# Kernel optimization log

Measured on AMD Instinct MI355X. Metric: run time of the kernel, lower is better.

## Reference

```python
import jax, jax.numpy as jnp
import numpy as np

N_NODES = 50000
N_HEADS = 8


def _make_edges(n, e_rand, seed=0):
    # unique random edges + self-loops so every row has >=1 neighbor
    rng = np.random.default_rng(seed)
    flat = rng.integers(0, n * n, size=e_rand, dtype=np.int64)
    flat = np.unique(np.concatenate([flat, np.arange(n, dtype=np.int64) * (n + 1)]))
    src = (flat // n).astype(np.int32)
    dst = (flat % n).astype(np.int32)
    return jnp.stack([jnp.asarray(src), jnp.asarray(dst)])


def setup_inputs() -> dict:
    key = jax.random.key(0)
    ks = jax.random.split(key, 10)
    d_in, d_att, d_out = 256, 64, 256
    dph = d_out // N_HEADS  # 32, per-head output dim of linearW
    s = 0.05
    return {
        "features": jax.random.normal(ks[0], (N_NODES, d_in), jnp.float32),
        "edge_index": _make_edges(N_NODES, 1_600_000),
        "Wq": jax.random.normal(ks[1], (N_HEADS, d_att, d_in), jnp.float32) * s,
        "bq": jax.random.normal(ks[2], (N_HEADS, d_att), jnp.float32) * s,
        "Wk": jax.random.normal(ks[3], (N_HEADS, d_att, d_in), jnp.float32) * s,
        "bk": jax.random.normal(ks[4], (N_HEADS, d_att), jnp.float32) * s,
        "Ww": jax.random.normal(ks[5], (dph, d_in), jnp.float32) * s,
        "bw": jax.random.normal(ks[6], (dph,), jnp.float32) * s,
        "Wb": jax.random.normal(ks[7], (d_out, d_in), jnp.float32) * s,
        "bb": jax.random.normal(ks[8], (d_out,), jnp.float32) * s,
    }


def reference(features, edge_index, Wq, bq, Wk, bk, Ww, bw, Wb, bb):
    n = features.shape[0]
    src, dst = edge_index[0], edge_index[1]
    # shared value projection (linearW is one layer reused for all heads)
    V = features @ Ww.T + bw  # [N, dph]
    head_outs = []
    for h in range(N_HEADS):  # structural loop over heads, as in the original
        q = features @ Wq[h].T + bq[h]  # [N, d_att]
        k = features @ Wk[h].T + bk[h]  # [N, d_att]
        s = jnp.sum(q[src] * k[dst], axis=-1)  # [E] = scores[i,j]=q_i.k_j on edges
        # row-wise (per source node) softmax over neighbors == dense masked softmax
        smax = jax.ops.segment_max(s, src, num_segments=n)
        ex = jnp.exp(s - jax.lax.stop_gradient(smax)[src])
        denom = jax.ops.segment_sum(ex, src, num_segments=n)
        alpha = ex / denom[src]  # [E]
        head_outs.append(jax.ops.segment_sum(alpha[:, None] * V[dst], src, num_segments=n))
    agg = jnp.concatenate(head_outs, axis=1)  # [N, d_out]
    return features @ Wb.T + bb + agg
```

## Files before the change

### kernel.cpp

```cpp
#include <hip/hip_runtime.h>
#include <hip/hip_fp16.h>

typedef _Float16 f16;
typedef _Float16 f16x2 __attribute__((ext_vector_type(2)));
typedef _Float16 f16x8 __attribute__((ext_vector_type(8)));
typedef float f32x4 __attribute__((ext_vector_type(4)));

#define WC_ROWS 1312
#define WC_PAD 1408

__global__ void prep_weights(const float* __restrict__ Wq, const float* __restrict__ bq,
                             const float* __restrict__ Wk, const float* __restrict__ bk,
                             const float* __restrict__ Ww, const float* __restrict__ bw,
                             const float* __restrict__ Wb, const float* __restrict__ bb,
                             f16* __restrict__ Wc, float* __restrict__ bias) {
    int id = blockIdx.x * 256 + threadIdx.x;
    int j = id >> 8, k = id & 255;
    if (j >= WC_PAD) return;
    float v;
    if (j < 512)       v = Wq[j*256 + k];
    else if (j < 1024) v = Wk[(j-512)*256 + k];
    else if (j < 1056) v = Ww[(j-1024)*256 + k];
    else if (j < 1312) v = Wb[(j-1056)*256 + k];
    else               v = 0.f;
    Wc[j*256 + k] = (f16)v;
    if (k == 0) {
        float b;
        if (j < 512)       b = bq[j];
        else if (j < 1024) b = bk[j-512];
        else if (j < 1056) b = bw[j-1024];
        else if (j < 1312) b = bb[j-1056];
        else               b = 0.f;
        bias[j] = b;
    }
}

__global__ void build_rows(const int* __restrict__ src, int E, int n, int* __restrict__ rs) {
    int e = blockIdx.x * 256 + threadIdx.x;
    if (e == 0) rs[n] = E;
    if (e < E) {
        if (e == 0 || src[e] != src[e-1]) rs[src[e]] = e;
    }
}

__device__ __forceinline__ int swz_slot(int row, int c) {
    return row * 4 + (c ^ (row & 3) ^ ((row >> 2) & 3));
}

__device__ __forceinline__ uint4 cvt8(float4 a, float4 b) {
    f16x8 o;
    o[0] = (f16)a.x; o[1] = (f16)a.y; o[2] = (f16)a.z; o[3] = (f16)a.w;
    o[4] = (f16)b.x; o[5] = (f16)b.y; o[6] = (f16)b.z; o[7] = (f16)b.w;
    return __builtin_bit_cast(uint4, o);
}

__launch_bounds__(256)
__global__ void gemm_fused(const float* __restrict__ F, const f16* __restrict__ Wc,
                           const float* __restrict__ bias,
                           f16* __restrict__ Qb, f16* __restrict__ Kb, f16* __restrict__ Vb,
                           float* __restrict__ Out, int n) {
    __shared__ uint4 As4[512];
    __shared__ uint4 Bs4[512];
    int t = threadIdx.x;
    int lane = t & 63, w = t >> 6;
    int wm = w >> 1, wn = w & 1;
    long m0 = (long)blockIdx.y * 128;
    int n0 = blockIdx.x * 128;

    f32x4 acc[4][4];
    #pragma unroll
    for (int i = 0; i < 4; i++)
        #pragma unroll
        for (int j = 0; j < 4; j++)
            acc[i][j] = (f32x4){0.f, 0.f, 0.f, 0.f};

    int lrow = t >> 2, lc = t & 3;
    long row0 = m0 + lrow, row1 = m0 + 64 + lrow;
    const float4* Fg0 = (const float4*)(F + row0 * 256 + lc * 8);
    const float4* Fg1 = (const float4*)(F + row1 * 256 + lc * 8);
    const uint4*  Bg0 = (const uint4*)(Wc + (long)(n0 + lrow) * 256 + lc * 8);
    const uint4*  Bg1 = (const uint4*)(Wc + (long)(n0 + 64 + lrow) * 256 + lc * 8);
    bool ok0 = row0 < n, ok1 = row1 < n;
    int ws0 = swz_slot(lrow, lc);
    int ws1 = swz_slot(lrow + 64, lc);
    int csw = (lane >> 4) ^ (lane & 3) ^ ((lane >> 2) & 3);
    int arow = wm * 64 + (lane & 15);
    int brow = wn * 64 + (lane & 15);

    float4 fa0 = {}, fb0 = {}, fa1 = {}, fb1 = {};
    if (ok0) { fa0 = Fg0[0]; fb0 = Fg0[1]; }
    if (ok1) { fa1 = Fg1[0]; fb1 = Fg1[1]; }
    uint4 rb0 = Bg0[0], rb1 = Bg1[0];
    for (int kt = 0; kt < 8; ++kt) {
        if (kt) __syncthreads();
        As4[ws0] = cvt8(fa0, fb0);
        As4[ws1] = cvt8(fa1, fb1);
        Bs4[ws0] = rb0;
        Bs4[ws1] = rb1;
        __syncthreads();
        if (kt < 7) {
            if (ok0) { fa0 = Fg0[(kt + 1) * 8]; fb0 = Fg0[(kt + 1) * 8 + 1]; }
            if (ok1) { fa1 = Fg1[(kt + 1) * 8]; fb1 = Fg1[(kt + 1) * 8 + 1]; }
            rb0 = Bg0[(kt + 1) * 4];
            rb1 = Bg1[(kt + 1) * 4];
        }
        f16x8 af[4], bf[4];
        const f16x8* Ap = (const f16x8*)As4;
        const f16x8* Bp = (const f16x8*)Bs4;
        #pragma unroll
        for (int i = 0; i < 4; i++) af[i] = Ap[(arow + i * 16) * 4 + csw];
        #pragma unroll
        for (int j = 0; j < 4; j++) bf[j] = Bp[(brow + j * 16) * 4 + csw];
        #pragma unroll
        for (int i = 0; i < 4; i++)
            #pragma unroll
            for (int j = 0; j < 4; j++)
                acc[i][j] = __builtin_amdgcn_mfma_f32_16x16x32_f16(af[i], bf[j], acc[i][j], 0, 0, 0);
    }

    #pragma unroll
    for (int i = 0; i < 4; i++) {
        long gmb = m0 + wm * 64 + i * 16 + (lane >> 4) * 4;
        #pragma unroll
        for (int j = 0; j < 4; j++) {
            int gn = n0 + wn * 64 + j * 16 + (lane & 15);
            float bv = bias[gn];
            #pragma unroll
            for (int r = 0; r < 4; r++) {
                long gm = gmb + r;
                if (gm >= n) continue;
                float v = acc[i][j][r] + bv;
                if (gn < 512)       Qb[gm * 512 + gn] = (f16)v;
                else if (gn < 1024) Kb[gm * 512 + (gn - 512)] = (f16)v;
                else if (gn < 1056) Vb[gm * 32 + (gn - 1024)] = (f16)v;
                else if (gn < 1312) Out[gm * 256 + (gn - 1056)] = v;
            }
        }
    }
}

__device__ __forceinline__ float fd2(unsigned a, unsigned b, float c) {
#if defined(__has_builtin)
#if __has_builtin(__builtin_amdgcn_fdot2)
    return __builtin_amdgcn_fdot2(__builtin_bit_cast(f16x2, a), __builtin_bit_cast(f16x2, b), c, false);
#else
    f16x2 x = __builtin_bit_cast(f16x2, a), y = __builtin_bit_cast(f16x2, b);
    return c + (float)x[0] * (float)y[0] + (float)x[1] * (float)y[1];
#endif
#else
    f16x2 x = __builtin_bit_cast(f16x2, a), y = __builtin_bit_cast(f16x2, b);
    return c + (float)x[0] * (float)y[0] + (float)x[1] * (float)y[1];
#endif
}

__launch_bounds__(256)
__global__ void edge_scores(const int* __restrict__ srcA, const int* __restrict__ dstA,
                            const f16* __restrict__ Qb, const f16* __restrict__ Kb,
                            f16* __restrict__ sE, int E, int Epad) {
    int bid = blockIdx.x;
    int h = bid & 7;
    int j = threadIdx.x & 7;
    int g = threadIdx.x >> 3;
    int e0 = (bid >> 3) * 128 + g;
    int s[4], d[4];
    #pragma unroll
    for (int u = 0; u < 4; u++) {
        int e = e0 + 32 * u;
        bool ok = e < E;
        s[u] = ok ? srcA[e] : 0;
        d[u] = ok ? dstA[e] : 0;
    }
    uint4 kv[4], qv[4];
    #pragma unroll
    for (int u = 0; u < 4; u++)
        kv[u] = *(const uint4*)(Kb + (size_t)d[u] * 512 + h * 64 + j * 8);
    #pragma unroll
    for (int u = 0; u < 4; u++)
        qv[u] = *(const uint4*)(Qb + (size_t)s[u] * 512 + h * 64 + j * 8);
    #pragma unroll
    for (int u = 0; u < 4; u++) {
        float a = 0.f;
        a = fd2(qv[u].x, kv[u].x, a);
        a = fd2(qv[u].y, kv[u].y, a);
        a = fd2(qv[u].z, kv[u].z, a);
        a = fd2(qv[u].w, kv[u].w, a);
        a += __shfl_xor(a, 1);
        a += __shfl_xor(a, 2);
        a += __shfl_xor(a, 4);
        int e = e0 + 32 * u;
        if (j == 0 && e < E)
            sE[(size_t)h * Epad + e] = (f16)a;
    }
}

__launch_bounds__(256)
__global__ void edge_agg(const int* __restrict__ rs, const int* __restrict__ dstA,
                         const f16* __restrict__ sE, const f16* __restrict__ Vb,
                         float* __restrict__ Out, int n, int Epad) {
    __shared__ __align__(16) f16 P_lds[4][16][64];
    __shared__ int dS[4][64];
    int w = threadIdx.x >> 6, lane = threadIdx.x & 63;
    int row = blockIdx.x * 4 + w;
    if (row >= n) return;
    int e0 = rs[row], deg = rs[row + 1] - e0;
    {
        f16x8 z = {};
        *(f16x8*)&P_lds[w][8 + (lane >> 3)][(lane & 7) * 8] = z;
    }
    asm volatile("" ::: "memory");
    float pm[8];
    #pragma unroll
    for (int h = 0; h < 8; h++) pm[h] = -1e30f;
    for (int base = 0; base < deg; base += 64) {
        bool act = lane < deg - base;
        int ee = e0 + base + (act ? lane : 0);
        #pragma unroll
        for (int h = 0; h < 8; h++) {
            float sv = act ? (float)sE[(size_t)h * Epad + ee] : -1e30f;
            pm[h] = fmaxf(pm[h], sv);
        }
    }
    float m[8];
    #pragma unroll
    for (int h = 0; h < 8; h++) {
        float v = pm[h];
        #pragma unroll
        for (int off = 1; off < 64; off <<= 1) v = fmaxf(v, __shfl_xor(v, off));
        m[h] = v;
    }
    f32x4 acc0 = {}, acc1 = {}, accl = {};
    int ec0 = (lane >> 4) * 8, h_a = lane & 15, hsel = (lane >> 4) & 1;
    f16x8 ones;
    #pragma unroll
    for (int j = 0; j < 8; j++) ones[j] = (f16)1.f;
    for (int base = 0; base < deg; base += 64) {
        int nE = deg - base; if (nE > 64) nE = 64;
        bool act = lane < nE;
        int ee = e0 + base + (act ? lane : 0);
        int d = dstA[ee];
        dS[w][lane] = d;
        #pragma unroll
        for (int h = 0; h < 8; h++) {
            float sv = act ? (float)sE[(size_t)h * Epad + ee] : 0.f;
            float p = act ? __expf(sv - m[h]) : 0.f;
            P_lds[w][h][lane ^ (h << 3)] = (f16)p;
        }
        asm volatile("" ::: "memory");
        f16x8 a0 = *(const f16x8*)&P_lds[w][h_a][(ec0)      ^ ((h_a & 7) << 3)];
        f16x8 a1 = *(const f16x8*)&P_lds[w][h_a][(32 + ec0) ^ ((h_a & 7) << 3)];
        f16x8 bf0a, bf0b, bf1a, bf1b;
        #pragma unroll
        for (int j = 0; j < 8; j++) {
            int dd0 = dS[w][ec0 + j];
            int dd1 = dS[w][32 + ec0 + j];
            const f16* vp0 = Vb + (size_t)dd0 * 32 + (lane & 15);
            const f16* vp1 = Vb + (size_t)dd1 * 32 + (lane & 15);
            bf0a[j] = vp0[0];  bf0b[j] = vp0[16];
            bf1a[j] = vp1[0];  bf1b[j] = vp1[16];
        }
        asm volatile("" ::: "memory");
        acc0 = __builtin_amdgcn_mfma_f32_16x16x32_f16(a0, bf0a, acc0, 0, 0, 0);
        acc0 = __builtin_amdgcn_mfma_f32_16x16x32_f16(a1, bf1a, acc0, 0, 0, 0);
        acc1 = __builtin_amdgcn_mfma_f32_16x16x32_f16(a0, bf0b, acc1, 0, 0, 0);
        acc1 = __builtin_amdgcn_mfma_f32_16x16x32_f16(a1, bf1b, acc1, 0, 0, 0);
        accl = __builtin_amdgcn_mfma_f32_16x16x32_f16(a0, ones, accl, 0, 0, 0);
        accl = __builtin_amdgcn_mfma_f32_16x16x32_f16(a1, ones, accl, 0, 0, 0);
    }
    if (lane < 32) {
        float* op = Out + (size_t)row * 256 + (lane & 15);
        #pragma unroll
        for (int r = 0; r < 4; r++) {
            int h = hsel * 4 + r;
            float inv = 1.f / accl[r];
            op[h * 32]      += acc0[r] * inv;
            op[h * 32 + 16] += acc1[r] * inv;
        }
    }
}

extern "C" void kernel_launch(void* const* d_in, const int* in_sizes, int n_in,
                              void* d_out, int out_size, void* d_ws, size_t ws_size,
                              hipStream_t stream) {
    const float* F  = (const float*)d_in[0];
    const int*   ei = (const int*)d_in[1];
    const float* Wq = (const float*)d_in[2];
    const float* bq = (const float*)d_in[3];
    const float* Wk = (const float*)d_in[4];
    const float* bk = (const float*)d_in[5];
    const float* Ww = (const float*)d_in[6];
    const float* bw = (const float*)d_in[7];
    const float* Wb = (const float*)d_in[8];
    const float* bb = (const float*)d_in[9];
    int n = in_sizes[0] / 256;
    int E = in_sizes[1] / 2;
    const int* srcA = ei;
    const int* dstA = ei + E;
    int n_pad = (n + 127) & ~127;
    int Epad = (E + 63) & ~63;

    char* wp = (char*)d_ws;
    auto alloc = [&](size_t bytes) { void* p = wp; wp += (bytes + 255) & ~255ull; return p; };
    f16*   sE   = (f16*)alloc((size_t)Epad * 8 * 2);
    f16*   Wc   = (f16*)alloc((size_t)WC_PAD * 256 * 2);
    float* bias = (float*)alloc((size_t)WC_PAD * 4);
    f16*   Qb   = (f16*)alloc((size_t)n * 512 * 2);
    f16*   Kb   = (f16*)alloc((size_t)n * 512 * 2);
    f16*   Vb   = (f16*)alloc((size_t)n * 32 * 2);
    int*   rs   = (int*)alloc((size_t)(n + 1) * 4);
    float* Out  = (float*)d_out;

    prep_weights<<<WC_PAD, 256, 0, stream>>>(Wq, bq, Wk, bk, Ww, bw, Wb, bb, Wc, bias);
    build_rows<<<(E + 255) / 256, 256, 0, stream>>>(srcA, E, n, rs);
    dim3 g(WC_PAD / 128, n_pad / 128);
    gemm_fused<<<g, 256, 0, stream>>>(F, Wc, bias, Qb, Kb, Vb, Out, n);
    int wgph = (E + 127) / 128;
    edge_scores<<<8 * wgph, 256, 0, stream>>>(srcA, dstA, Qb, Kb, sE, E, Epad);
    edge_agg<<<(n + 3) / 4, 256, 0, stream>>>(rs, dstA, sE, Vb, Out, n, Epad);
}
```

Before: 456.0 us.

## Use online softmax in edge aggregation and pack score reductions as f16x2

The edge aggregation kernel no longer makes a separate pass over the edge scores to find the per-row max. It switches to an online softmax that updates a running max per 64-edge chunk and rescales the accumulators by exp(m_old - m_new). This removes one full read of sE per row, at the cost of extra exponentials, accumulator rescaling and wave-wide max shuffles inside every chunk. Separately, the score kernel packs four per-edge partial dot products into two f16x2 registers and reduces them together, cutting shuffle count but summing the partials in half precision instead of fp32.

Measured after the change: 449.5 us. About the same (-1.4%).

```diff
diff --git a/kernel.cpp b/kernel.cpp
--- a/kernel.cpp
+++ b/kernel.cpp
@@ -177,6 +177,7 @@
     #pragma unroll
     for (int u = 0; u < 4; u++)
         qv[u] = *(const uint4*)(Qb + (size_t)s[u] * 512 + h * 64 + j * 8);
+    float aa[4];
     #pragma unroll
     for (int u = 0; u < 4; u++) {
         float a = 0.f;
@@ -184,12 +185,30 @@
         a = fd2(qv[u].y, kv[u].y, a);
         a = fd2(qv[u].z, kv[u].z, a);
         a = fd2(qv[u].w, kv[u].w, a);
-        a += __shfl_xor(a, 1);
-        a += __shfl_xor(a, 2);
-        a += __shfl_xor(a, 4);
-        int e = e0 + 32 * u;
-        if (j == 0 && e < E)
-            sE[(size_t)h * Epad + e] = (f16)a;
+        aa[u] = a;
+    }
+    f16x2 p01, p23;
+    p01[0] = (f16)aa[0]; p01[1] = (f16)aa[1];
+    p23[0] = (f16)aa[2]; p23[1] = (f16)aa[3];
+    unsigned u01 = __builtin_bit_cast(unsigned, p01);
+    unsigned u23 = __builtin_bit_cast(unsigned, p23);
+    #pragma unroll
+    for (int off = 1; off < 8; off <<= 1) {
+        unsigned v01 = __shfl_xor(u01, off);
+        unsigned v23 = __shfl_xor(u23, off);
+        f16x2 r01 = __builtin_bit_cast(f16x2, u01) + __builtin_bit_cast(f16x2, v01);
+        f16x2 r23 = __builtin_bit_cast(f16x2, u23) + __builtin_bit_cast(f16x2, v23);
+        u01 = __builtin_bit_cast(unsigned, r01);
+        u23 = __builtin_bit_cast(unsigned, r23);
+    }
+    if (j == 0) {
+        f16x2 r01 = __builtin_bit_cast(f16x2, u01);
+        f16x2 r23 = __builtin_bit_cast(f16x2, u23);
+        size_t bo = (size_t)h * Epad;
+        if (e0 < E)      sE[bo + e0]      = r01[0];
+        if (e0+32 < E)   sE[bo + e0+32]   = r01[1];
+        if (e0+64 < E)   sE[bo + e0+64]   = r23[0];
+        if (e0+96 < E)   sE[bo + e0+96]   = r23[1];
     }
 }
 
@@ -208,42 +227,39 @@
         *(f16x8*)&P_lds[w][8 + (lane >> 3)][(lane & 7) * 8] = z;
     }
     asm volatile("" ::: "memory");
-    float pm[8];
-    #pragma unroll
-    for (int h = 0; h < 8; h++) pm[h] = -1e30f;
-    for (int base = 0; base < deg; base += 64) {
-        bool act = lane < deg - base;
-        int ee = e0 + base + (act ? lane : 0);
-        #pragma unroll
-        for (int h = 0; h < 8; h++) {
-            float sv = act ? (float)sE[(size_t)h * Epad + ee] : -1e30f;
-            pm[h] = fmaxf(pm[h], sv);
-        }
-    }
     float m[8];
     #pragma unroll
-    for (int h = 0; h < 8; h++) {
-        float v = pm[h];
-        #pragma unroll
-        for (int off = 1; off < 64; off <<= 1) v = fmaxf(v, __shfl_xor(v, off));
-        m[h] = v;
-    }
+    for (int h = 0; h < 8; h++) m[h] = -1e30f;
     f32x4 acc0 = {}, acc1 = {}, accl = {};
     int ec0 = (lane >> 4) * 8, h_a = lane & 15, hsel = (lane >> 4) & 1;
     f16x8 ones;
     #pragma unroll
     for (int j = 0; j < 8; j++) ones[j] = (f16)1.f;
+
     for (int base = 0; base < deg; base += 64) {
         int nE = deg - base; if (nE > 64) nE = 64;
         bool act = lane < nE;
         int ee = e0 + base + (act ? lane : 0);
-        int d = dstA[ee];
-        dS[w][lane] = d;
+        dS[w][lane] = dstA[ee];
+        float sc[8];
         #pragma unroll
         for (int h = 0; h < 8; h++) {
-            float sv = act ? (float)sE[(size_t)h * Epad + ee] : 0.f;
-            float p = act ? __expf(sv - m[h]) : 0.f;
+            float sv = act ? (float)sE[(size_t)h * Epad + ee] : -1e30f;
+            float tv = sv;
+            #pragma unroll
+            for (int off = 1; off < 64; off <<= 1) tv = fmaxf(tv, __shfl_xor(tv, off));
+            float nm = fmaxf(m[h], tv);
+            sc[h] = __expf(m[h] - nm);
+            float p = act ? __expf(sv - nm) : 0.f;
             P_lds[w][h][lane ^ (h << 3)] = (f16)p;
+            m[h] = nm;
+        }
+        #pragma unroll
+        for (int r = 0; r < 4; r++) {
+            float f = hsel ? sc[r + 4] : sc[r];
+            acc0[r] *= f;
+            acc1[r] *= f;
+            accl[r] *= f;
         }
         asm volatile("" ::: "memory");
         f16x8 a0 = *(const f16x8*)&P_lds[w][h_a][(ec0)      ^ ((h_a & 7) << 3)];
```
